# Optimization experiments

Hardware: AMD Instinct MI355X
Metric: run time of the kernel (lower is better)

The kernel has to match this reference:

```python
import jax, jax.numpy as jnp
import numpy as np

IMG_H, IMG_W = 1024, 1024
TWO_PI = 2.0 * np.pi


def _pe_encoding(coords_norm, gauss):
    # coords_norm: [..., 2] in [0,1]
    c = 2.0 * coords_norm - 1.0
    c = (c @ gauss) * TWO_PI  # [..., num_pos_feats]
    return jnp.concatenate([jnp.sin(c), jnp.cos(c)], axis=-1)  # [..., embed_dim]


def setup_inputs() -> dict:
    key = jax.random.key(0)
    ks = jax.random.split(key, 9)
    B, N, D = 2048, 128, 256
    points = jax.random.uniform(ks[0], (B, N, 2), dtype=jnp.float32) * 1024.0
    labels = jax.random.randint(ks[1], (B, N), -1, 2, dtype=jnp.int32)  # {-1,0,1}
    boxes = jax.random.uniform(ks[2], (B, 4), dtype=jnp.float32) * 1024.0
    gauss = jax.random.normal(ks[3], (2, D // 2), dtype=jnp.float32)  # scale=1.0
    pe0 = jax.random.normal(ks[4], (D,), dtype=jnp.float32)
    pe1 = jax.random.normal(ks[5], (D,), dtype=jnp.float32)
    pe2 = jax.random.normal(ks[6], (D,), dtype=jnp.float32)
    pe3 = jax.random.normal(ks[7], (D,), dtype=jnp.float32)
    nap = jax.random.normal(ks[8], (D,), dtype=jnp.float32)
    return {"points": points, "labels": labels, "boxes": boxes, "gauss": gauss,
            "pe0": pe0, "pe1": pe1, "pe2": pe2, "pe3": pe3, "nap": nap}


def reference(points, labels, boxes, gauss, pe0, pe1, pe2, pe3, nap):
    inv_size = jnp.asarray([1.0 / IMG_W, 1.0 / IMG_H], dtype=points.dtype)

    # --- _embed_points (pad=False since boxes are given) ---
    p = (points + 0.5) * inv_size  # normalize x by W, y by H
    point_emb = _pe_encoding(p, gauss)  # [B, N, D]
    lab = labels[..., None]  # [B, N, 1]
    delta = jnp.where(lab == -1, nap,
             jnp.where(lab == 1, pe0,
              jnp.where(lab == 0, pe1, jnp.zeros_like(nap))))
    point_emb = point_emb + delta

    # --- _embed_boxes ---
    b = (boxes + 0.5).reshape(boxes.shape[0], 2, 2) * inv_size
    corner_emb = _pe_encoding(b, gauss)  # [B, 2, D]
    corner_emb = corner_emb + jnp.stack([pe2, pe3], axis=0)  # broadcast over B
    box_emb = jnp.mean(corner_emb, axis=1, keepdims=True)  # [B, 1, D]

    combined = jnp.concatenate([point_emb, box_emb], axis=1)  # [B, N+1, D]
    return jnp.mean(combined, axis=1, keepdims=True)  # [B, 1, D]
```

## Files before the change

kernel.cpp:

```cpp
#include <hip/hip_runtime.h>


#define NFEAT 128
#define N_PTS 128

__device__ __forceinline__ float sin2pi(float t) { return __builtin_amdgcn_sinf(t); }
__device__ __forceinline__ float cos2pi(float t) { return __builtin_amdgcn_cosf(t); }
__device__ __forceinline__ float fract_(float t) { return __builtin_amdgcn_fractf(t); }
__device__ __forceinline__ float rdlane(float v, int l) {
    return __int_as_float(__builtin_amdgcn_readlane(__float_as_int(v), l));
}

__global__ __launch_bounds__(256)
void prompt_encoder_kernel(const float* __restrict__ points,
                           const int*   __restrict__ labels,
                           const float* __restrict__ boxes,
                           const float* __restrict__ gauss,
                           const float* __restrict__ pe0,
                           const float* __restrict__ pe1,
                           const float* __restrict__ pe2,
                           const float* __restrict__ pe3,
                           const float* __restrict__ nap,
                           float* __restrict__ out)
{
    const int b    = blockIdx.x;
    const int tid  = threadIdx.x;
    const int lane = tid & 63;
    const int w    = tid >> 6;
    const int jf   = (w & 1) * 64 + lane;
    const int h    = w >> 1;

    __shared__ float ps[4][64];
    __shared__ float pc[4][64];
    __shared__ int   scnt[6];

    float2 p = ((const float2*)points)[(size_t)b * N_PTS + h * 64 + lane];

    if (w < 2) {
        int lab = labels[(size_t)b * N_PTS + w * 64 + lane];
        unsigned long long bm1 = __ballot(lab == -1);
        unsigned long long bz  = __ballot(lab == 0);
        unsigned long long bp1 = __ballot(lab == 1);
        if (lane == 0) {
            scnt[w * 3 + 0] = __popcll(bm1);
            scnt[w * 3 + 1] = __popcll(bz);
            scnt[w * 3 + 2] = __popcll(bp1);
        }
    }

    const float a  = 1.0f / 512.0f;
    const float g0 = gauss[jf];
    const float g1 = gauss[NFEAT + jf];
    const float G0 = g0 * a, G1 = g1 * a;
    const float C  = (0.5f * a - 1.0f) * (g0 + g1);

    float ss0 = 0.f, ss1 = 0.f, cs0 = 0.f, cs1 = 0.f;
    #pragma unroll
    for (int l = 0; l < 64; l += 2) {
        float sx0 = rdlane(p.x, l),     sy0 = rdlane(p.y, l);
        float sx1 = rdlane(p.x, l + 1), sy1 = rdlane(p.y, l + 1);
        float t0 = fract_(fmaf(sx0, G0, fmaf(sy0, G1, C)));
        float t1 = fract_(fmaf(sx1, G0, fmaf(sy1, G1, C)));
        ss0 += sin2pi(t0); cs0 += cos2pi(t0);
        ss1 += sin2pi(t1); cs1 += cos2pi(t1);
    }
    ps[w][lane] = ss0 + ss1;
    pc[w][lane] = cs0 + cs1;
    __syncthreads();

    const int d   = tid;
    const int j   = d & (NFEAT - 1);
    const int wlo = j >> 6;
    const int li  = j & 63;
    float sum = (d < NFEAT) ? (ps[wlo][li] + ps[wlo + 2][li])
                            : (pc[wlo][li] + pc[wlo + 2][li]);

    float cm1 = (float)(scnt[0] + scnt[3]);
    float c0n = (float)(scnt[1] + scnt[4]);
    float cp1 = (float)(scnt[2] + scnt[5]);
    float delv = cm1 * nap[d] + cp1 * pe0[d] + c0n * pe1[d];

    float gg0 = gauss[j], gg1 = gauss[NFEAT + j];
    float4 bx = ((const float4*)boxes)[b];
    float t0 = fract_(fmaf((bx.x + 0.5f) * a - 1.0f, gg0,
                           ((bx.y + 0.5f) * a - 1.0f) * gg1));
    float t1 = fract_(fmaf((bx.z + 0.5f) * a - 1.0f, gg0,
                           ((bx.w + 0.5f) * a - 1.0f) * gg1));
    float tr0, tr1;
    if (d < NFEAT) { tr0 = sin2pi(t0); tr1 = sin2pi(t1); }
    else           { tr0 = cos2pi(t0); tr1 = cos2pi(t1); }
    float box = 0.5f * ((tr0 + pe2[d]) + (tr1 + pe3[d]));

    out[(size_t)b * 256 + d] = (sum + delv + box) * (1.0f / (float)(N_PTS + 1));
}

extern "C" void kernel_launch(void* const* d_in, const int* in_sizes, int n_in,
                              void* d_out, int out_size, void* d_ws, size_t ws_size,
                              hipStream_t stream) {
    const float* points = (const float*)d_in[0];
    const int*   labels = (const int*)d_in[1];
    const float* boxes  = (const float*)d_in[2];
    const float* gauss  = (const float*)d_in[3];
    const float* pe0    = (const float*)d_in[4];
    const float* pe1    = (const float*)d_in[5];
    const float* pe2    = (const float*)d_in[6];
    const float* pe3    = (const float*)d_in[7];
    const float* nap    = (const float*)d_in[8];
    float* out = (float*)d_out;

    const int B = in_sizes[2] / 4;

    prompt_encoder_kernel<<<B, 256, 0, stream>>>(points, labels, boxes, gauss,
                                                 pe0, pe1, pe2, pe3, nap, out);
}
```

Before: 16.50 us.

## Stage points in LDS and use packed FMA for two features per thread

Restructures the point loop so each thread handles two features (f and f+64) over a quarter of the points read from shared memory, replacing readlane broadcasts with LDS loads and computing both phases with one pair of v_pk_fma_f32 instructions. The fract range-reduction calls are removed, relying on the hardware sin/cos accepting unreduced input, and the final reduction sums four partials. This cuts scalar readlane work and halves the FMA count, at the cost of an extra barrier, LDS traffic and reliance on the hardware trig range for accuracy.

```diff
diff --git a/kernel.cpp b/kernel.cpp
--- a/kernel.cpp
+++ b/kernel.cpp
@@ -4,11 +4,22 @@
 #define NFEAT 128
 #define N_PTS 128
 
+typedef float v2f __attribute__((ext_vector_type(2)));
+
 __device__ __forceinline__ float sin2pi(float t) { return __builtin_amdgcn_sinf(t); }
 __device__ __forceinline__ float cos2pi(float t) { return __builtin_amdgcn_cosf(t); }
-__device__ __forceinline__ float fract_(float t) { return __builtin_amdgcn_fractf(t); }
-__device__ __forceinline__ float rdlane(float v, int l) {
-    return __int_as_float(__builtin_amdgcn_readlane(__float_as_int(v), l));
+
+__device__ __forceinline__ v2f pk_fma_bcast_y(v2f c, v2f s1, v2f s2) {
+    v2f d;
+    asm("v_pk_fma_f32 %0, %1, %2, %3 op_sel:[1,0,0]"
+        : "=v"(d) : "v"(c), "v"(s1), "v"(s2));
+    return d;
+}
+__device__ __forceinline__ v2f pk_fma_bcast_x(v2f c, v2f s1, v2f s2) {
+    v2f d;
+    asm("v_pk_fma_f32 %0, %1, %2, %3 op_sel_hi:[0,1,1]"
+        : "=v"(d) : "v"(c), "v"(s1), "v"(s2));
+    return d;
 }
 
 __global__ __launch_bounds__(256)
@@ -23,57 +34,58 @@
                            const float* __restrict__ nap,
                            float* __restrict__ out)
 {
-    const int b    = blockIdx.x;
-    const int tid  = threadIdx.x;
-    const int lane = tid & 63;
-    const int w    = tid >> 6;
-    const int jf   = (w & 1) * 64 + lane;
-    const int h    = w >> 1;
+    const int b   = blockIdx.x;
+    const int tid = threadIdx.x;
+    const int f   = tid & 63;
+    const int q   = tid >> 6;
 
-    __shared__ float ps[4][64];
-    __shared__ float pc[4][64];
+    __shared__ v2f   sc[N_PTS];
+    __shared__ float ps[4][NFEAT];
+    __shared__ float pc[4][NFEAT];
     __shared__ int   scnt[6];
 
-    float2 p = ((const float2*)points)[(size_t)b * N_PTS + h * 64 + lane];
+    ((float*)sc)[tid] = (points + (size_t)b * 2 * N_PTS)[tid];
 
-    if (w < 2) {
-        int lab = labels[(size_t)b * N_PTS + w * 64 + lane];
+    if (q < 2) {
+        int lab = labels[(size_t)b * N_PTS + q * 64 + (tid & 63)];
         unsigned long long bm1 = __ballot(lab == -1);
         unsigned long long bz  = __ballot(lab == 0);
         unsigned long long bp1 = __ballot(lab == 1);
-        if (lane == 0) {
-            scnt[w * 3 + 0] = __popcll(bm1);
-            scnt[w * 3 + 1] = __popcll(bz);
-            scnt[w * 3 + 2] = __popcll(bp1);
+        if ((tid & 63) == 0) {
+            scnt[q * 3 + 0] = __popcll(bm1);
+            scnt[q * 3 + 1] = __popcll(bz);
+            scnt[q * 3 + 2] = __popcll(bp1);
         }
     }
 
-    const float a  = 1.0f / 512.0f;
-    const float g0 = gauss[jf];
-    const float g1 = gauss[NFEAT + jf];
-    const float G0 = g0 * a, G1 = g1 * a;
-    const float C  = (0.5f * a - 1.0f) * (g0 + g1);
+    const float a    = 1.0f / 512.0f;
+    const float coff = 0.5f * a - 1.0f;
+    const float g0l = gauss[f],        g0h = gauss[f + 64];
+    const float g1l = gauss[NFEAT + f], g1h = gauss[NFEAT + f + 64];
+    v2f G0p; G0p.x = g0l * a;  G0p.y = g0h * a;
+    v2f G1p; G1p.x = g1l * a;  G1p.y = g1h * a;
+    v2f Cp;  Cp.x  = coff * (g0l + g1l); Cp.y = coff * (g0h + g1h);
 
-    float ss0 = 0.f, ss1 = 0.f, cs0 = 0.f, cs1 = 0.f;
-    #pragma unroll
-    for (int l = 0; l < 64; l += 2) {
-        float sx0 = rdlane(p.x, l),     sy0 = rdlane(p.y, l);
-        float sx1 = rdlane(p.x, l + 1), sy1 = rdlane(p.y, l + 1);
-        float t0 = fract_(fmaf(sx0, G0, fmaf(sy0, G1, C)));
-        float t1 = fract_(fmaf(sx1, G0, fmaf(sy1, G1, C)));
-        ss0 += sin2pi(t0); cs0 += cos2pi(t0);
-        ss1 += sin2pi(t1); cs1 += cos2pi(t1);
-    }
-    ps[w][lane] = ss0 + ss1;
-    pc[w][lane] = cs0 + cs1;
     __syncthreads();
 
-    const int d   = tid;
-    const int j   = d & (NFEAT - 1);
-    const int wlo = j >> 6;
-    const int li  = j & 63;
-    float sum = (d < NFEAT) ? (ps[wlo][li] + ps[wlo + 2][li])
-                            : (pc[wlo][li] + pc[wlo + 2][li]);
+    float ssl = 0.f, csl = 0.f, ssh = 0.f, csh = 0.f;
+    const v2f* scq = &sc[q * 32];
+    #pragma unroll
+    for (int n = 0; n < 32; ++n) {
+        v2f c  = scq[n];
+        v2f u  = pk_fma_bcast_y(c, G1p, Cp);
+        v2f t2 = pk_fma_bcast_x(c, G0p, u);
+        ssl += sin2pi(t2.x); csl += cos2pi(t2.x);
+        ssh += sin2pi(t2.y); csh += cos2pi(t2.y);
+    }
+    ps[q][f] = ssl; ps[q][f + 64] = ssh;
+    pc[q][f] = csl; pc[q][f + 64] = csh;
+    __syncthreads();
+
+    const int d = tid;
+    const int j = d & (NFEAT - 1);
+    float sum = (d < NFEAT) ? (ps[0][j] + ps[1][j] + ps[2][j] + ps[3][j])
+                            : (pc[0][j] + pc[1][j] + pc[2][j] + pc[3][j]);
 
     float cm1 = (float)(scnt[0] + scnt[3]);
     float c0n = (float)(scnt[1] + scnt[4]);
@@ -82,10 +94,8 @@
 
     float gg0 = gauss[j], gg1 = gauss[NFEAT + j];
     float4 bx = ((const float4*)boxes)[b];
-    float t0 = fract_(fmaf((bx.x + 0.5f) * a - 1.0f, gg0,
-                           ((bx.y + 0.5f) * a - 1.0f) * gg1));
-    float t1 = fract_(fmaf((bx.z + 0.5f) * a - 1.0f, gg0,
-                           ((bx.w + 0.5f) * a - 1.0f) * gg1));
+    float t0 = fmaf(fmaf(bx.x, a, coff), gg0, fmaf(bx.y, a, coff) * gg1);
+    float t1 = fmaf(fmaf(bx.z, a, coff), gg0, fmaf(bx.w, a, coff) * gg1);
     float tr0, tr1;
     if (d < NFEAT) { tr0 = sin2pi(t0); tr1 = sin2pi(t1); }
     else           { tr0 = cos2pi(t0); tr1 = cos2pi(t1); }
```

After: 13.69 us. 1.21x faster.
